# Kernel tuning notes

Hardware: AMD Instinct MI355X
Metric: run time of the kernel (lower is better)

Reference implementation:

```python
import jax, jax.numpy as jnp
import numpy as np

IN_F = 4096
OUT_F = 4096
SPLIT_F = 410   # ceil(4096 * 0.1)
NUM_PARTS = 10  # ceil(4096 / 410)


def setup_inputs() -> dict:
    key = jax.random.key(0)
    ks = jax.random.split(key, 7)
    s = 1.0 / np.sqrt(IN_F)
    sn = 1.0 / np.sqrt(NUM_PARTS)
    return {
        'x': jax.random.normal(ks[0], (2, 2048, IN_F), dtype=jnp.float32),
        'Wsel': jax.random.uniform(ks[1], (NUM_PARTS, IN_F), jnp.float32, -s, s),
        'bsel': jax.random.uniform(ks[2], (NUM_PARTS,), jnp.float32, -s, s),
        'Wexp': jax.random.uniform(ks[3], (IN_F, NUM_PARTS), jnp.float32, -sn, sn),
        'bexp': jax.random.uniform(ks[4], (IN_F,), jnp.float32, -sn, sn),
        'Wfc': jax.random.uniform(ks[5], (SPLIT_F, IN_F), jnp.float32, -s, s),
        'bfc': jax.random.uniform(ks[6], (SPLIT_F,), jnp.float32, -s, s),
        'out_features': OUT_F,
    }


def reference(x, Wsel, bsel, Wexp, bexp, Wfc, bfc, out_features):
    # selector: sx[..., n]
    sx = jnp.einsum('bsi,ni->bsn', x, Wsel) + bsel
    # expander(diag_embed(sx)): px[..., n, f] = sx[..., n] * Wexp[f, n] + bexp[f]
    # (diag matrix never materialized; mathematically identical)
    px = sx[..., :, None] * Wexp.T[None, None, :, :] + bexp  # [b, s, n, in]
    xx = x[..., None, :] + px                                # broadcast-add of x
    y = jnp.einsum('bsni,fi->bsnf', xx, Wfc) + bfc           # splitfc, [b, s, n, sf]
    y = y.reshape(y.shape[0], y.shape[1], -1)                # (n sf) flatten
    return y[..., :out_features]
```

## Files before the change

### kernel.cpp

```cpp
#include <hip/hip_runtime.h>
#include <hip/hip_bf16.h>
#include <stdint.h>

#define TKS    4096
#define KD     4096
#define NSF    410
#define NPARTS 10
#define OUTF   4096

#define BM 32
#define BN 64
#define BK 64

typedef unsigned short u16;
typedef __attribute__((ext_vector_type(8))) short bf16x8;
typedef __attribute__((ext_vector_type(4))) float f32x4;

#define WS_XB  0
#define WS_BSW ((size_t)TKS * KD * 2)
#define WS_WSL (WS_BSW + (size_t)512 * KD * 2)
#define WS_WEX (WS_WSL + (size_t)16 * KD * 2)

__device__ inline u16 f2bf(float f) {
    union { __hip_bfloat16 b; u16 u; } cv;
    cv.b = __float2bfloat16(f);
    return cv.u;
}

typedef __attribute__((address_space(3))) unsigned int as3_uint;
typedef __attribute__((address_space(1))) unsigned int as1_uint;
__device__ inline void gl_lds16(const void* g, void* l) {
    __builtin_amdgcn_global_load_lds((as1_uint*)(uintptr_t)g,
                                     (as3_uint*)(uintptr_t)l, 16, 0, 0);
}

__device__ inline int g_row(int g) { int s = g >> 6; return (s >> 2) * 32 + (s & 1) * 16 + (g & 15); }
__device__ inline int g_col(int g) { int s = g >> 6; return ((s >> 1) & 1) * 32 + ((g >> 4) & 3) * 8; }

__global__ __launch_bounds__(256) void prep_w(const float* __restrict__ Wsel,
                                              const float* __restrict__ Wexp,
                                              const float* __restrict__ bexp,
                                              u16* __restrict__ wselb,
                                              u16* __restrict__ wexpb) {
    const int kt = blockIdx.x;
    const int tid = threadIdx.x;
    const int g  = tid & 127;
    const int ml = g & 15;
    const int col = kt * 64 + (g >> 6) * 32 + ((g >> 4) & 3) * 8;
    u16 h[8];
    if (tid < 128) {
#pragma unroll
        for (int j = 0; j < 8; ++j)
            h[j] = (ml < NPARTS) ? f2bf(Wsel[(size_t)ml * KD + col + j]) : (u16)0;
        *(uint4*)&wselb[((size_t)kt * 128 + g) * 8] = *(uint4*)h;
    } else {
#pragma unroll
        for (int j = 0; j < 8; ++j)
            h[j] = (ml < NPARTS) ? f2bf(Wexp[(size_t)(col + j) * NPARTS + ml])
                 : (ml == NPARTS ? f2bf(bexp[col + j]) : (u16)0);
        *(uint4*)&wexpb[((size_t)kt * 128 + g) * 8] = *(uint4*)h;
    }
}

__global__ __launch_bounds__(256) void retile_b(const float* __restrict__ Wfc,
                                                u16* __restrict__ bsw) {
    const int kt = blockIdx.x & 63, rb = blockIdx.x >> 6;
    const int tid = threadIdx.x;
    u16* tout = bsw + ((size_t)(rb * 64 + kt) * 512) * 8;
#pragma unroll
    for (int j = 0; j < 2; ++j) {
        const int g = j * 256 + tid;
        const int r = rb * 64 + g_row(g);
        uint4 pk = make_uint4(0u, 0u, 0u, 0u);
        if (r < NSF) {
            const float* src = Wfc + (size_t)r * KD + kt * 64 + g_col(g);
            float4 v0 = *(const float4*)src;
            float4 v1 = *(const float4*)(src + 4);
            u16 h[8] = { f2bf(v0.x), f2bf(v0.y), f2bf(v0.z), f2bf(v0.w),
                         f2bf(v1.x), f2bf(v1.y), f2bf(v1.z), f2bf(v1.w) };
            pk = *(uint4*)h;
        }
        *(uint4*)&tout[(size_t)g * 8] = pk;
    }
}

__global__ __launch_bounds__(256) void retile_x(const float* __restrict__ x,
                                                u16* __restrict__ xb) {
    const int kt = blockIdx.x & 63, tb = blockIdx.x >> 6;
    const int g = threadIdx.x;
    const int slot = g >> 6;
    const int row = (slot & 1) * 16 + (g & 15);
    const int col = (slot >> 1) * 32 + ((g >> 4) & 3) * 8;
    const float* src = x + (size_t)(tb * 32 + row) * KD + kt * 64 + col;
    float4 v0 = *(const float4*)src;
    float4 v1 = *(const float4*)(src + 4);
    u16 h[8] = { f2bf(v0.x), f2bf(v0.y), f2bf(v0.z), f2bf(v0.w),
                 f2bf(v1.x), f2bf(v1.y), f2bf(v1.z), f2bf(v1.w) };
    *(uint4*)&xb[((size_t)(tb * 64 + kt) * 256 + g) * 8] = *(uint4*)h;
}

__global__ __launch_bounds__(256, 4) void main_kernel(const u16* __restrict__ xb,
                                                      const u16* __restrict__ bsw,
                                                      const u16* __restrict__ wselb,
                                                      const u16* __restrict__ wexpb,
                                                      const float* __restrict__ bsel,
                                                      const float* __restrict__ bfc,
                                                      float* __restrict__ out) {
    __shared__ __align__(16) u16 As[2][2048];
    __shared__ __align__(16) u16 Bs[2][4096];
    __shared__ __align__(16) u16 Wl[2][1024];
    __shared__ __align__(16) u16 We[2][1024];
    __shared__ float sxs[BM][NPARTS];
    __shared__ float Gs[BN][NPARTS];
    __shared__ float cs[BN];

    const int tid = threadIdx.x;
    const int fb  = blockIdx.x >> 7;
    const int tb  = blockIdx.x & 127;

    const int lane = tid & 63;
    const int w  = tid >> 6;
    const int mt = w & 1, wc = w >> 1;
    const int q  = lane >> 4, ml = lane & 15;

    f32x4 acc[2]   = { (f32x4){0.f,0.f,0.f,0.f}, (f32x4){0.f,0.f,0.f,0.f} };
    f32x4 accsx    = (f32x4){0.f,0.f,0.f,0.f};
    f32x4 accG[2]  = { (f32x4){0.f,0.f,0.f,0.f}, (f32x4){0.f,0.f,0.f,0.f} };

    const u16* ab = xb  + (size_t)tb * 131072;
    const u16* bb = bsw + (size_t)fb * 262144;

    gl_lds16(ab + tid * 8, &As[0][tid * 8]);
    gl_lds16(bb + tid * 8, &Bs[0][tid * 8]);
    gl_lds16(bb + (256 + tid) * 8, &Bs[0][(256 + tid) * 8]);
    if (tid < 128) gl_lds16(wselb + tid * 8, &Wl[0][tid * 8]);
    else           gl_lds16(wexpb + (tid - 128) * 8, &We[0][(tid - 128) * 8]);
    __syncthreads();

    int buf = 0;
#pragma unroll 2
    for (int it = 0; it < KD / BK; ++it) {
        if (it + 1 < KD / BK) {
            const size_t ao = (size_t)(it + 1) * 2048;
            const size_t bo = (size_t)(it + 1) * 4096;
            const size_t wo = (size_t)(it + 1) * 1024;
            gl_lds16(ab + ao + tid * 8, &As[buf ^ 1][tid * 8]);
            gl_lds16(bb + bo + tid * 8, &Bs[buf ^ 1][tid * 8]);
            gl_lds16(bb + bo + (256 + tid) * 8, &Bs[buf ^ 1][(256 + tid) * 8]);
            if (tid < 128) gl_lds16(wselb + wo + tid * 8, &Wl[buf ^ 1][tid * 8]);
            else           gl_lds16(wexpb + wo + (tid - 128) * 8, &We[buf ^ 1][(tid - 128) * 8]);
        }
#pragma unroll
        for (int ks = 0; ks < 2; ++ks) {
            bf16x8 av  = *(const bf16x8*)&As[buf][((ks * 2 + mt) * 64 + lane) * 8];
            bf16x8 bv0 = *(const bf16x8*)&Bs[buf][((wc * 4 + ks * 2 + 0) * 64 + lane) * 8];
            bf16x8 bv1 = *(const bf16x8*)&Bs[buf][((wc * 4 + ks * 2 + 1) * 64 + lane) * 8];
            acc[0] = __builtin_amdgcn_mfma_f32_16x16x32_bf16(av, bv0, acc[0], 0, 0, 0);
            acc[1] = __builtin_amdgcn_mfma_f32_16x16x32_bf16(av, bv1, acc[1], 0, 0, 0);
            if (wc == 0) {
                bf16x8 wf = *(const bf16x8*)&Wl[buf][(ks * 64 + lane) * 8];
                accsx = __builtin_amdgcn_mfma_f32_16x16x32_bf16(av, wf, accsx, 0, 0, 0);
            }
            if (mt == 0) {
                bf16x8 ef = *(const bf16x8*)&We[buf][(ks * 64 + lane) * 8];
                accG[0] = __builtin_amdgcn_mfma_f32_16x16x32_bf16(bv0, ef, accG[0], 0, 0, 0);
                accG[1] = __builtin_amdgcn_mfma_f32_16x16x32_bf16(bv1, ef, accG[1], 0, 0, 0);
            }
        }
        __syncthreads();
        buf ^= 1;
    }

    if (wc == 0 && ml < NPARTS) {
        const float bs = bsel[ml];
#pragma unroll
        for (int r = 0; r < 4; ++r)
            sxs[mt * 16 + q * 4 + r][ml] = accsx[r] + bs;
    }
    if (mt == 0) {
#pragma unroll
        for (int ni = 0; ni < 2; ++ni) {
#pragma unroll
            for (int r = 0; r < 4; ++r) {
                const int f = wc * 32 + ni * 16 + q * 4 + r;
                if (ml < NPARTS) Gs[f][ml] = accG[ni][r];
                else if (ml == NPARTS) {
                    const int fg = fb * BN + f;
                    cs[f] = accG[ni][r] + (fg < NSF ? bfc[fg] : 0.f);
                }
            }
        }
    }
    __syncthreads();

#pragma unroll
    for (int ni = 0; ni < 2; ++ni) {
        const int fl = wc * 32 + ni * 16 + ml;
        const int fg = fb * BN + fl;
        if (fg >= NSF) continue;
        const float cv = cs[fl];
        float gv[NPARTS];
#pragma unroll
        for (int n = 0; n < NPARTS; ++n) gv[n] = Gs[fl][n];
#pragma unroll
        for (int r = 0; r < 4; ++r) {
            const int tl = mt * 16 + q * 4 + r;
            const float av = acc[ni][r] + cv;
            float* orow = out + (size_t)(tb * BM + tl) * OUTF;
#pragma unroll
            for (int n = 0; n < NPARTS; ++n) {
                int j = n * NSF + fg;
                if (j < OUTF) orow[j] = av + sxs[tl][n] * gv[n];
            }
        }
    }
}

extern "C" void kernel_launch(void* const* d_in, const int* in_sizes, int n_in,
                              void* d_out, int out_size, void* d_ws, size_t ws_size,
                              hipStream_t stream) {
    const float* x    = (const float*)d_in[0];
    const float* Wsel = (const float*)d_in[1];
    const float* bsel = (const float*)d_in[2];
    const float* Wexp = (const float*)d_in[3];
    const float* bexp = (const float*)d_in[4];
    const float* Wfc  = (const float*)d_in[5];
    const float* bfc  = (const float*)d_in[6];
    float* out = (float*)d_out;

    char* ws = (char*)d_ws;
    u16* xb    = (u16*)(ws + WS_XB);
    u16* bsw   = (u16*)(ws + WS_BSW);
    u16* wselb = (u16*)(ws + WS_WSL);
    u16* wexpb = (u16*)(ws + WS_WEX);

    prep_w<<<dim3(64), dim3(256), 0, stream>>>(Wsel, Wexp, bexp, wselb, wexpb);
    retile_b<<<dim3(7 * 64), dim3(256), 0, stream>>>(Wfc, bsw);
    retile_x<<<dim3(128 * 64), dim3(256), 0, stream>>>(x, xb);
    main_kernel<<<dim3(7 * 128), dim3(256), 0, stream>>>(xb, bsw, wselb, wexpb,
                                                         bsel, bfc, out);
}
```

Measured before the change: 200.2 us.

## Alias epilogue LDS onto staging buffers and use fine-grained vmcnt waits

Packs all shared buffers into one 32KB array, with the epilogue scratch (sxs, Gs, cs) aliased onto the double-buffered staging area. This cuts LDS per block so launch bounds can request 5 blocks per CU instead of 4. It also replaces the __syncthreads pair with explicit s_waitcnt vmcnt(4)/lgkmcnt(0) plus raw s_barrier, so the prefetch of the next tile stays in flight while the current one is consumed. The hand-counted vmcnt value depends on how many loads each thread issues, and the extra occupancy may force register spills.

```diff
diff --git a/kernel.cpp b/kernel.cpp
--- a/kernel.cpp
+++ b/kernel.cpp
@@ -99,20 +99,21 @@
     *(uint4*)&xb[((size_t)(tb * 64 + kt) * 256 + g) * 8] = *(uint4*)h;
 }
 
-__global__ __launch_bounds__(256, 4) void main_kernel(const u16* __restrict__ xb,
+__global__ __launch_bounds__(256, 5) void main_kernel(const u16* __restrict__ xb,
                                                       const u16* __restrict__ bsw,
                                                       const u16* __restrict__ wselb,
                                                       const u16* __restrict__ wexpb,
                                                       const float* __restrict__ bsel,
                                                       const float* __restrict__ bfc,
                                                       float* __restrict__ out) {
-    __shared__ __align__(16) u16 As[2][2048];
-    __shared__ __align__(16) u16 Bs[2][4096];
-    __shared__ __align__(16) u16 Wl[2][1024];
-    __shared__ __align__(16) u16 We[2][1024];
-    __shared__ float sxs[BM][NPARTS];
-    __shared__ float Gs[BN][NPARTS];
-    __shared__ float cs[BN];
+    __shared__ __align__(16) u16 smem[16384];
+    u16* const Asb = smem;
+    u16* const Bsb = smem + 4096;
+    u16* const Wlb = smem + 12288;
+    u16* const Web = smem + 14336;
+    float* const sxs = (float*)smem;
+    float* const Gs  = (float*)(smem + 640);
+    float* const cs  = (float*)(smem + 1920);
 
     const int tid = threadIdx.x;
     const int fb  = blockIdx.x >> 7;
@@ -130,52 +131,60 @@
     const u16* ab = xb  + (size_t)tb * 131072;
     const u16* bb = bsw + (size_t)fb * 262144;
 
-    gl_lds16(ab + tid * 8, &As[0][tid * 8]);
-    gl_lds16(bb + tid * 8, &Bs[0][tid * 8]);
-    gl_lds16(bb + (256 + tid) * 8, &Bs[0][(256 + tid) * 8]);
-    if (tid < 128) gl_lds16(wselb + tid * 8, &Wl[0][tid * 8]);
-    else           gl_lds16(wexpb + (tid - 128) * 8, &We[0][(tid - 128) * 8]);
-    __syncthreads();
-
-    int buf = 0;
+#define STAGE(it1, nb) do {                                                      \
+        const size_t ao_ = (size_t)(it1) * 2048;                                 \
+        const size_t bo_ = (size_t)(it1) * 4096;                                 \
+        const size_t wo_ = (size_t)(it1) * 1024;                                 \
+        gl_lds16(ab + ao_ + tid * 8,        &Asb[(nb) * 2048 + tid * 8]);        \
+        gl_lds16(bb + bo_ + tid * 8,        &Bsb[(nb) * 4096 + tid * 8]);        \
+        gl_lds16(bb + bo_ + (256 + tid) * 8,&Bsb[(nb) * 4096 + (256 + tid) * 8]);\
+        if (tid < 128) gl_lds16(wselb + wo_ + tid * 8,                           \
+                                &Wlb[(nb) * 1024 + tid * 8]);                    \
+        else           gl_lds16(wexpb + wo_ + (tid - 128) * 8,                   \
+                                &Web[(nb) * 1024 + (tid - 128) * 8]);            \
+    } while (0)
+
+    STAGE(0, 0);
+
 #pragma unroll 2
     for (int it = 0; it < KD / BK; ++it) {
+        const int buf = it & 1;
         if (it + 1 < KD / BK) {
-            const size_t ao = (size_t)(it + 1) * 2048;
-            const size_t bo = (size_t)(it + 1) * 4096;
-            const size_t wo = (size_t)(it + 1) * 1024;
-            gl_lds16(ab + ao + tid * 8, &As[buf ^ 1][tid * 8]);
-            gl_lds16(bb + bo + tid * 8, &Bs[buf ^ 1][tid * 8]);
-            gl_lds16(bb + bo + (256 + tid) * 8, &Bs[buf ^ 1][(256 + tid) * 8]);
-            if (tid < 128) gl_lds16(wselb + wo + tid * 8, &Wl[buf ^ 1][tid * 8]);
-            else           gl_lds16(wexpb + wo + (tid - 128) * 8, &We[buf ^ 1][(tid - 128) * 8]);
-        }
+            STAGE(it + 1, buf ^ 1);
+            asm volatile("s_waitcnt vmcnt(4)" ::: "memory");
+        } else {
+            asm volatile("s_waitcnt vmcnt(0)" ::: "memory");
+        }
+        __builtin_amdgcn_s_barrier();
+        asm volatile("" ::: "memory");
 #pragma unroll
         for (int ks = 0; ks < 2; ++ks) {
-            bf16x8 av  = *(const bf16x8*)&As[buf][((ks * 2 + mt) * 64 + lane) * 8];
-            bf16x8 bv0 = *(const bf16x8*)&Bs[buf][((wc * 4 + ks * 2 + 0) * 64 + lane) * 8];
-            bf16x8 bv1 = *(const bf16x8*)&Bs[buf][((wc * 4 + ks * 2 + 1) * 64 + lane) * 8];
+            bf16x8 av  = *(const bf16x8*)&Asb[buf * 2048 + ((ks * 2 + mt) * 64 + lane) * 8];
+            bf16x8 bv0 = *(const bf16x8*)&Bsb[buf * 4096 + ((wc * 4 + ks * 2 + 0) * 64 + lane) * 8];
+            bf16x8 bv1 = *(const bf16x8*)&Bsb[buf * 4096 + ((wc * 4 + ks * 2 + 1) * 64 + lane) * 8];
             acc[0] = __builtin_amdgcn_mfma_f32_16x16x32_bf16(av, bv0, acc[0], 0, 0, 0);
             acc[1] = __builtin_amdgcn_mfma_f32_16x16x32_bf16(av, bv1, acc[1], 0, 0, 0);
             if (wc == 0) {
-                bf16x8 wf = *(const bf16x8*)&Wl[buf][(ks * 64 + lane) * 8];
+                bf16x8 wf = *(const bf16x8*)&Wlb[buf * 1024 + (ks * 64 + lane) * 8];
                 accsx = __builtin_amdgcn_mfma_f32_16x16x32_bf16(av, wf, accsx, 0, 0, 0);
             }
             if (mt == 0) {
-                bf16x8 ef = *(const bf16x8*)&We[buf][(ks * 64 + lane) * 8];
+                bf16x8 ef = *(const bf16x8*)&Web[buf * 1024 + (ks * 64 + lane) * 8];
                 accG[0] = __builtin_amdgcn_mfma_f32_16x16x32_bf16(bv0, ef, accG[0], 0, 0, 0);
                 accG[1] = __builtin_amdgcn_mfma_f32_16x16x32_bf16(bv1, ef, accG[1], 0, 0, 0);
             }
         }
-        __syncthreads();
-        buf ^= 1;
-    }
+        asm volatile("s_waitcnt lgkmcnt(0)" ::: "memory");
+        __builtin_amdgcn_s_barrier();
+        asm volatile("" ::: "memory");
+    }
+#undef STAGE
 
     if (wc == 0 && ml < NPARTS) {
         const float bs = bsel[ml];
 #pragma unroll
         for (int r = 0; r < 4; ++r)
-            sxs[mt * 16 + q * 4 + r][ml] = accsx[r] + bs;
+            sxs[(mt * 16 + q * 4 + r) * NPARTS + ml] = accsx[r] + bs;
     }
     if (mt == 0) {
 #pragma unroll
@@ -183,7 +192,7 @@
 #pragma unroll
             for (int r = 0; r < 4; ++r) {
                 const int f = wc * 32 + ni * 16 + q * 4 + r;
-                if (ml < NPARTS) Gs[f][ml] = accG[ni][r];
+                if (ml < NPARTS) Gs[f * NPARTS + ml] = accG[ni][r];
                 else if (ml == NPARTS) {
                     const int fg = fb * BN + f;
                     cs[f] = accG[ni][r] + (fg < NSF ? bfc[fg] : 0.f);
@@ -201,7 +210,7 @@
         const float cv = cs[fl];
         float gv[NPARTS];
 #pragma unroll
-        for (int n = 0; n < NPARTS; ++n) gv[n] = Gs[fl][n];
+        for (int n = 0; n < NPARTS; ++n) gv[n] = Gs[fl * NPARTS + n];
 #pragma unroll
         for (int r = 0; r < 4; ++r) {
             const int tl = mt * 16 + q * 4 + r;
@@ -210,7 +219,7 @@
 #pragma unroll
             for (int n = 0; n < NPARTS; ++n) {
                 int j = n * NSF + fg;
-                if (j < OUTF) orow[j] = av + sxs[tl][n] * gv[n];
+                if (j < OUTF) orow[j] = av + sxs[tl * NPARTS + n] * gv[n];
             }
         }
     }
```

Result: no change. 201.5 us (+0.6%).

## Split selector/expander GEMMs into separate kernel and use split-K register-fed main GEMM

Applied to the files above, without the earlier changes.

Moves the small sx (x·Wsel) and G (Wfc·Wexp) products into a new sel_g kernel that writes them to workspace, so the main kernel no longer spends MFMAs and LDS on them. The main kernel now drops LDS double-buffering and loads fragments straight from global memory into registers with software prefetch. Each block covers a 64x32 tile, and its four waves split K four ways, with the partial sums reduced through LDS. This adds a kernel launch, a workspace round-trip and a split-K reduction, and the direct global loads may have lower reuse than the old LDS tiling.

```diff
diff --git a/kernel.cpp b/kernel.cpp
--- a/kernel.cpp
+++ b/kernel.cpp
@@ -8,16 +8,14 @@
 #define NPARTS 10
 #define OUTF   4096
 
-#define BM 32
-#define BN 64
-#define BK 64
-
 typedef unsigned short u16;
 typedef __attribute__((ext_vector_type(8))) short bf16x8;
 typedef __attribute__((ext_vector_type(4))) float f32x4;
 
 #define WS_XB  0
 #define WS_BSW ((size_t)TKS * KD * 2)
+#define WS_SX  (WS_BSW + (size_t)448 * 512 * 8 * 2)
+#define WS_GC  (WS_SX + (size_t)TKS * NPARTS * 4)
 #define WS_WSL (WS_BSW + (size_t)512 * KD * 2)
 #define WS_WEX (WS_WSL + (size_t)16 * KD * 2)
 
@@ -25,13 +23,6 @@
     union { __hip_bfloat16 b; u16 u; } cv;
     cv.b = __float2bfloat16(f);
     return cv.u;
-}
-
-typedef __attribute__((address_space(3))) unsigned int as3_uint;
-typedef __attribute__((address_space(1))) unsigned int as1_uint;
-__device__ inline void gl_lds16(const void* g, void* l) {
-    __builtin_amdgcn_global_load_lds((as1_uint*)(uintptr_t)g,
-                                     (as3_uint*)(uintptr_t)l, 16, 0, 0);
 }
 
 __device__ inline int g_row(int g) { int s = g >> 6; return (s >> 2) * 32 + (s & 1) * 16 + (g & 15); }
@@ -99,118 +90,170 @@
     *(uint4*)&xb[((size_t)(tb * 64 + kt) * 256 + g) * 8] = *(uint4*)h;
 }
 
+__global__ __launch_bounds__(256) void sel_g(const u16* __restrict__ xb,
+                                             const u16* __restrict__ bsw,
+                                             const u16* __restrict__ wselb,
+                                             const u16* __restrict__ wexpb,
+                                             const float* __restrict__ bsel,
+                                             const float* __restrict__ bfc,
+                                             float* __restrict__ sxb,
+                                             float* __restrict__ gc) {
+    __shared__ float lred[4][64][16];
+    const int tid = threadIdx.x, lane = tid & 63, w = tid >> 6;
+    const int q = lane >> 4, ml = lane & 15;
+    const int b = blockIdx.x;
+
+    if (b < 128) {
+        f32x4 a0 = (f32x4){0.f,0.f,0.f,0.f}, a1 = (f32x4){0.f,0.f,0.f,0.f};
+        for (int kt = w * 16; kt < w * 16 + 16; ++kt) {
+#pragma unroll
+            for (int ks = 0; ks < 2; ++ks) {
+                bf16x8 wl  = *(const bf16x8*)&wselb[((size_t)kt * 128 + ks * 64 + lane) * 8];
+                bf16x8 av0 = *(const bf16x8*)&xb[(((size_t)b * 64 + kt) * 256 + (ks * 2 + 0) * 64 + lane) * 8];
+                bf16x8 av1 = *(const bf16x8*)&xb[(((size_t)b * 64 + kt) * 256 + (ks * 2 + 1) * 64 + lane) * 8];
+                a0 = __builtin_amdgcn_mfma_f32_16x16x32_bf16(av0, wl, a0, 0, 0, 0);
+                a1 = __builtin_amdgcn_mfma_f32_16x16x32_bf16(av1, wl, a1, 0, 0, 0);
+            }
+        }
+#pragma unroll
+        for (int r = 0; r < 4; ++r) {
+            lred[w][q * 4 + r][ml]      = a0[r];
+            lred[w][16 + q * 4 + r][ml] = a1[r];
+        }
+        __syncthreads();
+        for (int i = tid; i < 32 * NPARTS; i += 256) {
+            const int t = i / NPARTS, n = i % NPARTS;
+            sxb[((size_t)b * 32 + t) * NPARTS + n] =
+                lred[0][t][n] + lred[1][t][n] + lred[2][t][n] + lred[3][t][n] + bsel[n];
+        }
+    } else {
+        const int fb = b - 128;
+        f32x4 g0 = (f32x4){0.f,0.f,0.f,0.f}, g1 = g0, g2 = g0, g3 = g0;
+        for (int kt = w * 16; kt < w * 16 + 16; ++kt) {
+#pragma unroll
+            for (int ks = 0; ks < 2; ++ks) {
+                bf16x8 ef = *(const bf16x8*)&wexpb[((size_t)kt * 128 + ks * 64 + lane) * 8];
+                bf16x8 b0 = *(const bf16x8*)&bsw[(((size_t)fb * 64 + kt) * 512 + (0 * 4 + ks * 2 + 0) * 64 + lane) * 8];
+                bf16x8 b1 = *(const bf16x8*)&bsw[(((size_t)fb * 64 + kt) * 512 + (0 * 4 + ks * 2 + 1) * 64 + lane) * 8];
+                bf16x8 b2 = *(const bf16x8*)&bsw[(((size_t)fb * 64 + kt) * 512 + (1 * 4 + ks * 2 + 0) * 64 + lane) * 8];
+                bf16x8 b3 = *(const bf16x8*)&bsw[(((size_t)fb * 64 + kt) * 512 + (1 * 4 + ks * 2 + 1) * 64 + lane) * 8];
+                g0 = __builtin_amdgcn_mfma_f32_16x16x32_bf16(b0, ef, g0, 0, 0, 0);
+                g1 = __builtin_amdgcn_mfma_f32_16x16x32_bf16(b1, ef, g1, 0, 0, 0);
+                g2 = __builtin_amdgcn_mfma_f32_16x16x32_bf16(b2, ef, g2, 0, 0, 0);
+                g3 = __builtin_amdgcn_mfma_f32_16x16x32_bf16(b3, ef, g3, 0, 0, 0);
+            }
+        }
+#pragma unroll
+        for (int r = 0; r < 4; ++r) {
+            lred[w][ 0 + q * 4 + r][ml] = g0[r];
+            lred[w][16 + q * 4 + r][ml] = g1[r];
+            lred[w][32 + q * 4 + r][ml] = g2[r];
+            lred[w][48 + q * 4 + r][ml] = g3[r];
+        }
+        __syncthreads();
+        for (int i = tid; i < 64 * 11; i += 256) {
+            const int f = i / 11, c = i % 11;
+            float s = lred[0][f][c] + lred[1][f][c] + lred[2][f][c] + lred[3][f][c];
+            const int fg = fb * 64 + f;
+            if (c == 10) s += (fg < NSF ? bfc[fg] : 0.f);
+            gc[(size_t)fg * 12 + c] = s;
+        }
+    }
+}
+
+#define A_IDX(kt, mi, ks) ((((size_t)(tb * 2 + ((mi) >> 1)) * 64 + (size_t)(kt)) * 256 \
+                            + ((ks) * 2 + ((mi) & 1)) * 64 + lane) * 8)
+#define B_IDX(kt, nj, ks) (((size_t)(fb * 64 + (kt)) * 512 \
+                            + (wf * 4 + (ks) * 2 + (nj)) * 64 + lane) * 8)
+
 __global__ __launch_bounds__(256, 4) void main_kernel(const u16* __restrict__ xb,
                                                       const u16* __restrict__ bsw,
-                                                      const u16* __restrict__ wselb,
-                                                      const u16* __restrict__ wexpb,
-                                                      const float* __restrict__ bsel,
-                                                      const float* __restrict__ bfc,
+                                                      const float* __restrict__ sxb,
+                                                      const float* __restrict__ gc,
                                                       float* __restrict__ out) {
-    __shared__ __align__(16) u16 As[2][2048];
-    __shared__ __align__(16) u16 Bs[2][4096];
-    __shared__ __align__(16) u16 Wl[2][1024];
-    __shared__ __align__(16) u16 We[2][1024];
-    __shared__ float sxs[BM][NPARTS];
-    __shared__ float Gs[BN][NPARTS];
-    __shared__ float cs[BN];
+    __shared__ float red[4][4][16][34];
+    __shared__ float sxt[64][NPARTS];
+    __shared__ float gt[32][12];
 
     const int tid = threadIdx.x;
-    const int fb  = blockIdx.x >> 7;
-    const int tb  = blockIdx.x & 127;
-
+    const int f2 = blockIdx.x >> 6;
+    const int tb = blockIdx.x & 63;
     const int lane = tid & 63;
-    const int w  = tid >> 6;
-    const int mt = w & 1, wc = w >> 1;
-    const int q  = lane >> 4, ml = lane & 15;
-
-    f32x4 acc[2]   = { (f32x4){0.f,0.f,0.f,0.f}, (f32x4){0.f,0.f,0.f,0.f} };
-    f32x4 accsx    = (f32x4){0.f,0.f,0.f,0.f};
-    f32x4 accG[2]  = { (f32x4){0.f,0.f,0.f,0.f}, (f32x4){0.f,0.f,0.f,0.f} };
-
-    const u16* ab = xb  + (size_t)tb * 131072;
-    const u16* bb = bsw + (size_t)fb * 262144;
-
-    gl_lds16(ab + tid * 8, &As[0][tid * 8]);
-    gl_lds16(bb + tid * 8, &Bs[0][tid * 8]);
-    gl_lds16(bb + (256 + tid) * 8, &Bs[0][(256 + tid) * 8]);
-    if (tid < 128) gl_lds16(wselb + tid * 8, &Wl[0][tid * 8]);
-    else           gl_lds16(wexpb + (tid - 128) * 8, &We[0][(tid - 128) * 8]);
+    const int kh = tid >> 6;
+    const int q = lane >> 4, ml = lane & 15;
+    const int fb = f2 >> 1, wf = f2 & 1;
+
+    f32x4 acc[4][2];
+#pragma unroll
+    for (int mi = 0; mi < 4; ++mi)
+#pragma unroll
+        for (int nj = 0; nj < 2; ++nj) acc[mi][nj] = (f32x4){0.f,0.f,0.f,0.f};
+
+    bf16x8 fa[2][4], fbv[2][2];
+
+#define LOADAB(p, kt, ks) do {                                            \
+        _Pragma("unroll")                                                 \
+        for (int mi = 0; mi < 4; ++mi)                                    \
+            fa[p][mi] = *(const bf16x8*)&xb[A_IDX((kt), mi, (ks))];       \
+        _Pragma("unroll")                                                 \
+        for (int nj = 0; nj < 2; ++nj)                                    \
+            fbv[p][nj] = *(const bf16x8*)&bsw[B_IDX((kt), nj, (ks))];     \
+    } while (0)
+
+#define MFMAS(p) do {                                                     \
+        _Pragma("unroll")                                                 \
+        for (int mi = 0; mi < 4; ++mi)                                    \
+            _Pragma("unroll")                                             \
+            for (int nj = 0; nj < 2; ++nj)                                \
+                acc[mi][nj] = __builtin_amdgcn_mfma_f32_16x16x32_bf16(    \
+                    fa[p][mi], fbv[p][nj], acc[mi][nj], 0, 0, 0);         \
+    } while (0)
+
+    LOADAB(0, kh * 16, 0);
+    for (int it2 = 0; it2 < 16; ++it2) {
+        const int kt = kh * 16 + it2;
+        LOADAB(1, kt, 1);
+        MFMAS(0);
+        if (it2 + 1 < 16) LOADAB(0, kt + 1, 0);
+        MFMAS(1);
+    }
+#undef LOADAB
+#undef MFMAS
+
+#pragma unroll
+    for (int mi = 0; mi < 4; ++mi)
+#pragma unroll
+        for (int nj = 0; nj < 2; ++nj)
+#pragma unroll
+            for (int r = 0; r < 4; ++r)
+                red[mi][kh][q * 4 + r][nj * 16 + ml] = acc[mi][nj][r];
+
+    for (int i = tid; i < 64 * NPARTS; i += 256)
+        sxt[i / NPARTS][i % NPARTS] = sxb[((size_t)tb * 64 + i / NPARTS) * NPARTS + i % NPARTS];
+    for (int i = tid; i < 32 * 11; i += 256)
+        gt[i / 11][i % 11] = gc[((size_t)f2 * 32 + i / 11) * 12 + i % 11];
     __syncthreads();
 
-    int buf = 0;
-#pragma unroll 2
-    for (int it = 0; it < KD / BK; ++it) {
-        if (it + 1 < KD / BK) {
-            const size_t ao = (size_t)(it + 1) * 2048;
-            const size_t bo = (size_t)(it + 1) * 4096;
-            const size_t wo = (size_t)(it + 1) * 1024;
-            gl_lds16(ab + ao + tid * 8, &As[buf ^ 1][tid * 8]);
-            gl_lds16(bb + bo + tid * 8, &Bs[buf ^ 1][tid * 8]);
-            gl_lds16(bb + bo + (256 + tid) * 8, &Bs[buf ^ 1][(256 + tid) * 8]);
-            if (tid < 128) gl_lds16(wselb + wo + tid * 8, &Wl[buf ^ 1][tid * 8]);
-            else           gl_lds16(wexpb + wo + (tid - 128) * 8, &We[buf ^ 1][(tid - 128) * 8]);
-        }
-#pragma unroll
-        for (int ks = 0; ks < 2; ++ks) {
-            bf16x8 av  = *(const bf16x8*)&As[buf][((ks * 2 + mt) * 64 + lane) * 8];
-            bf16x8 bv0 = *(const bf16x8*)&Bs[buf][((wc * 4 + ks * 2 + 0) * 64 + lane) * 8];
-            bf16x8 bv1 = *(const bf16x8*)&Bs[buf][((wc * 4 + ks * 2 + 1) * 64 + lane) * 8];
-            acc[0] = __builtin_amdgcn_mfma_f32_16x16x32_bf16(av, bv0, acc[0], 0, 0, 0);
-            acc[1] = __builtin_amdgcn_mfma_f32_16x16x32_bf16(av, bv1, acc[1], 0, 0, 0);
-            if (wc == 0) {
-                bf16x8 wf = *(const bf16x8*)&Wl[buf][(ks * 64 + lane) * 8];
-                accsx = __builtin_amdgcn_mfma_f32_16x16x32_bf16(av, wf, accsx, 0, 0, 0);
-            }
-            if (mt == 0) {
-                bf16x8 ef = *(const bf16x8*)&We[buf][(ks * 64 + lane) * 8];
-                accG[0] = __builtin_amdgcn_mfma_f32_16x16x32_bf16(bv0, ef, accG[0], 0, 0, 0);
-                accG[1] = __builtin_amdgcn_mfma_f32_16x16x32_bf16(bv1, ef, accG[1], 0, 0, 0);
-            }
-        }
-        __syncthreads();
-        buf ^= 1;
-    }
-
-    if (wc == 0 && ml < NPARTS) {
-        const float bs = bsel[ml];
-#pragma unroll
-        for (int r = 0; r < 4; ++r)
-            sxs[mt * 16 + q * 4 + r][ml] = accsx[r] + bs;
-    }
-    if (mt == 0) {
-#pragma unroll
-        for (int ni = 0; ni < 2; ++ni) {
-#pragma unroll
-            for (int r = 0; r < 4; ++r) {
-                const int f = wc * 32 + ni * 16 + q * 4 + r;
-                if (ml < NPARTS) Gs[f][ml] = accG[ni][r];
-                else if (ml == NPARTS) {
-                    const int fg = fb * BN + f;
-                    cs[f] = accG[ni][r] + (fg < NSF ? bfc[fg] : 0.f);
-                }
-            }
-        }
-    }
-    __syncthreads();
-
-#pragma unroll
-    for (int ni = 0; ni < 2; ++ni) {
-        const int fl = wc * 32 + ni * 16 + ml;
-        const int fg = fb * BN + fl;
+#pragma unroll
+    for (int nj = 0; nj < 2; ++nj) {
+        const int fl = nj * 16 + ml;
+        const int fg = f2 * 32 + fl;
         if (fg >= NSF) continue;
-        const float cv = cs[fl];
+        const float cv = gt[fl][10];
         float gv[NPARTS];
 #pragma unroll
-        for (int n = 0; n < NPARTS; ++n) gv[n] = Gs[fl][n];
+        for (int n = 0; n < NPARTS; ++n) gv[n] = gt[fl][n];
 #pragma unroll
         for (int r = 0; r < 4; ++r) {
-            const int tl = mt * 16 + q * 4 + r;
-            const float av = acc[ni][r] + cv;
-            float* orow = out + (size_t)(tb * BM + tl) * OUTF;
+            const int tl = kh * 16 + q * 4 + r;
+            const float v = red[kh][0][q * 4 + r][fl] + red[kh][1][q * 4 + r][fl]
+                          + red[kh][2][q * 4 + r][fl] + red[kh][3][q * 4 + r][fl];
+            const float av = v + cv;
+            float* orow = out + (size_t)(tb * 64 + tl) * OUTF;
 #pragma unroll
             for (int n = 0; n < NPARTS; ++n) {
-                int j = n * NSF + fg;
-                if (j < OUTF) orow[j] = av + sxs[tl][n] * gv[n];
+                const int j = n * NSF + fg;
+                if (j < OUTF) orow[j] = av + sxt[tl][n] * gv[n];
             }
         }
     }
@@ -233,10 +276,12 @@
     u16* bsw   = (u16*)(ws + WS_BSW);
     u16* wselb = (u16*)(ws + WS_WSL);
     u16* wexpb = (u16*)(ws + WS_WEX);
+    float* sxb = (float*)(ws + WS_SX);
+    float* gcv = (float*)(ws + WS_GC);
 
     prep_w<<<dim3(64), dim3(256), 0, stream>>>(Wsel, Wexp, bexp, wselb, wexpb);
     retile_b<<<dim3(7 * 64), dim3(256), 0, stream>>>(Wfc, bsw);
     retile_x<<<dim3(128 * 64), dim3(256), 0, stream>>>(x, xb);
-    main_kernel<<<dim3(7 * 128), dim3(256), 0, stream>>>(xb, bsw, wselb, wexpb,
-                                                         bsel, bfc, out);
-}
+    sel_g<<<dim3(135), dim3(256), 0, stream>>>(xb, bsw, wselb, wexpb, bsel, bfc, sxb, gcv);
+    main_kernel<<<dim3(13 * 64), dim3(256), 0, stream>>>(xb, bsw, sxb, gcv, out);
+}
```

Result: slower. 215.7 us (+7.7%).
